# Kernel optimization log

Measured on AMD Instinct MI355X. Metric: run time of the kernel, lower is better.

## Reference

```python
import jax, jax.numpy as jnp
import numpy as np

CODEBOOK_SIZE = 1024
D_MODEL = 512
NUM_SAMPLES = 10
TEMP = 1.0
COMMITMENT_COST = 0.25
PADDING_IDX = 0


def setup_inputs() -> dict:
    key = jax.random.key(0)
    k1, k2, k3 = jax.random.split(key, 3)
    inputs = jax.random.normal(k1, (64, 512, D_MODEL), dtype=jnp.float32)
    padding_mask = jax.random.randint(k2, (64, 512), 0, 2) == 1
    codebook_weight = 0.02 * jax.random.normal(k3, (CODEBOOK_SIZE, D_MODEL), dtype=jnp.float32)
    codebook_weight = codebook_weight.at[PADDING_IDX].set(0.0)  # padding_idx row zeroed
    return {"inputs": inputs, "padding_mask": padding_mask, "codebook_weight": codebook_weight}


def reference(inputs, padding_mask, codebook_weight):
    B, S, D = inputs.shape
    K = codebook_weight.shape[0]
    flat = inputs.reshape(-1, D)  # [N, D]
    # squared-euclidean distances to codebook entries: [N, K]
    dist = (jnp.sum(flat * flat, axis=1, keepdims=True)
            + jnp.sum(codebook_weight * codebook_weight, axis=1)
            - 2.0 * (flat @ codebook_weight.T))
    pad = padding_mask.reshape(-1)  # [N]
    col = jnp.arange(K)
    # padded rows: only code 0 allowed; non-padded rows: code 0 disallowed
    allowed = jnp.where(pad[:, None], col == 0, col != 0)
    dist = jnp.where(allowed, dist, jnp.inf)

    # Multinomial(total_count=NUM_SAMPLES, logits=-dist/TEMP): draw NUM_SAMPLES
    # categorical samples per row and count them.
    logits = -dist / TEMP
    N = flat.shape[0]
    draws = jax.random.categorical(jax.random.key(42), logits, axis=-1,
                                   shape=(NUM_SAMPLES, N))  # [num_samples, N]
    row_idx = jnp.broadcast_to(jnp.arange(N)[None, :], draws.shape)
    samples = jnp.zeros((N, K), jnp.float32).at[row_idx, draws].add(1.0)  # counts, [N, K]

    quantized = (samples @ codebook_weight).reshape(B, S, D) / NUM_SAMPLES

    num_nonpad = (jnp.sum(~pad) * D).astype(jnp.float32)
    e_latent_loss = jnp.sum((jax.lax.stop_gradient(quantized) - inputs) ** 2) / num_nonpad
    loss = COMMITMENT_COST * e_latent_loss

    # straight-through estimator
    quantized_st = inputs + jax.lax.stop_gradient(quantized - inputs)

    avg_probs = jnp.mean(samples, axis=0) / NUM_SAMPLES  # [K]
    perplexity = jnp.exp(-jnp.sum(avg_probs * jnp.log(avg_probs + 1e-10)))

    samples_out = samples.reshape(B, S, K)
    return quantized_st, samples_out, loss, perplexity
```

## Files before the change

kernel.cpp:

```cpp
#include <hip/hip_runtime.h>
#include <stdint.h>

#define NROWS 32768
#define KC 1024
#define DM 512
#define NKPROD 33554432u

typedef _Float16 v8h __attribute__((ext_vector_type(8)));
typedef float v4f __attribute__((ext_vector_type(4)));

__device__ __forceinline__ uint32_t rotl32(uint32_t x, int d) {
  return __builtin_amdgcn_alignbit(x, x, 32 - d);
}

__device__ __forceinline__ void threefry_x2(uint32_t xa, uint32_t xb,
                                            uint32_t& oa, uint32_t& ob) {
  const uint32_t ks1 = 42u, ks2 = 0x1BD11BF0u;
  uint32_t a0 = 0u, a1 = xa + ks1;
  uint32_t b0 = 0u, b1 = xb + ks1;
#define R2(r) { a0 += a1; b0 += b1; a1 = rotl32(a1, r); b1 = rotl32(b1, r); a1 ^= a0; b1 ^= b0; }
  R2(13) R2(15) R2(26) R2(6)
  a0 += ks1; b0 += ks1; a1 += ks2 + 1u; b1 += ks2 + 1u;
  R2(17) R2(29) R2(16) R2(24)
  a0 += ks2; b0 += ks2; a1 += 2u; b1 += 2u;
  R2(13) R2(15) R2(26) R2(6)
  a1 += ks1 + 3u; b1 += ks1 + 3u;
  R2(17) R2(29) R2(16) R2(24)
  a0 += ks1; b0 += ks1; a1 += ks2 + 4u; b1 += ks2 + 4u;
  R2(13) R2(15) R2(26) R2(6)
  a0 += ks2; b0 += ks2; a1 += 5u; b1 += 5u;
#undef R2
  oa = a0 ^ a1;
  ob = b0 ^ b1;
}

__global__ __launch_bounds__(1024) void k_prep(const void* __restrict__ mv,
                                               uint8_t* __restrict__ wm,
                                               int* __restrict__ idx,
                                               int* __restrict__ npp) {
  __shared__ uint32_t sflag;
  __shared__ int scnt[1024];
  int t = threadIdx.x;
  if (t == 0) sflag = 0;
  __syncthreads();
  const uint8_t* mb = (const uint8_t*)mv;
  uint32_t f = 0;
  for (int i = t; i < NROWS; i += 1024)
    if ((i & 3) && mb[i]) f = 1;
  if (f) atomicOr(&sflag, 1u);
  __syncthreads();
  bool isbool = sflag != 0;

  int r0 = t * 32;
  int cnt = 0;
  for (int i = 0; i < 32; ++i) {
    int r = r0 + i;
    bool p = isbool ? (mb[r] != 0) : (((const int*)mv)[r] != 0);
    wm[r] = p ? 1u : 0u;
    cnt += p ? 0 : 1;
  }
  scnt[t] = cnt;
  __syncthreads();
  for (int off = 1; off < 1024; off <<= 1) {
    int v = (t >= off) ? scnt[t - off] : 0;
    __syncthreads();
    scnt[t] += v;
    __syncthreads();
  }
  int NPtot = scnt[1023];
  int pos  = scnt[t] - cnt;
  int ppos = NPtot + (r0 - pos);
  for (int i = 0; i < 32; ++i) {
    int r = r0 + i;
    bool p = isbool ? (mb[r] != 0) : (((const int*)mv)[r] != 0);
    if (!p) idx[pos++] = r; else idx[ppos++] = r;
  }
  if (t == 1023) *npp = NPtot;
}

__global__ __launch_bounds__(256) void k_bsplit(const float* __restrict__ B,
                                                _Float16* __restrict__ Bh2,
                                                _Float16* __restrict__ Bl2,
                                                float* __restrict__ Bn) {
  int k = blockIdx.x * 4 + (threadIdx.x >> 6);
  int l = threadIdx.x & 63;
  const float* bp = B + (size_t)k * DM + l * 8;
  float x[8];
  *(float4*)&x[0] = *(const float4*)bp;
  *(float4*)&x[4] = *(const float4*)(bp + 4);
  _Float16 h[8], lo[8];
  float s = 0.f;
#pragma unroll
  for (int i = 0; i < 8; ++i) {
    _Float16 hh = (_Float16)x[i];
    h[i] = hh; lo[i] = (_Float16)(x[i] - (float)hh);
    s = fmaf(x[i], x[i], s);
  }
  *(v8h*)&Bh2[(size_t)k * DM + l * 8] = *(v8h*)h;
  *(v8h*)&Bl2[(size_t)k * DM + l * 8] = *(v8h*)lo;
#pragma unroll
  for (int off = 32; off; off >>= 1) s += __shfl_xor(s, off, 64);
  if (l == 0) Bn[k] = s;
}

#define LDK 40
__global__ __launch_bounds__(256) void k_gemm3(const float* __restrict__ A,
                                               const _Float16* __restrict__ Bh2,
                                               const _Float16* __restrict__ Bl2,
                                               const float* __restrict__ Bn,
                                               const int* __restrict__ idx,
                                               const int* __restrict__ npp,
                                               float* __restrict__ S) {
  int NP = *npp;
  int bx = blockIdx.x & 7;
  int by = blockIdx.x >> 3;
  int r0 = by * 128, c0 = bx * 128;
  if (r0 >= NP) return;

  __shared__ _Float16 Ah[128 * LDK], Al[128 * LDK];
  __shared__ _Float16 Bh[128 * LDK], Bl[128 * LDK];
  __shared__ float rs[128];
  __shared__ float cs[128];
  __shared__ float tmp[256];

  int tid = threadIdx.x;
  int wid = tid >> 6;
  int wr = wid >> 1, wc = wid & 1;
  int l = tid & 63;
  int lr = l & 15;
  int k8 = (l >> 4) * 8;

  int srow = tid >> 1;
  int ssub = (tid & 1) * 16;

  int orig = idx[r0 + srow];
  const float* ag = A + (size_t)orig * DM + ssub;
  const _Float16* bhg = Bh2 + (size_t)(c0 + srow) * DM + ssub;
  const _Float16* blg = Bl2 + (size_t)(c0 + srow) * DM + ssub;

  if (tid < 128) cs[tid] = Bn[c0 + tid];

  v4f acc[4][4];
#pragma unroll
  for (int m = 0; m < 4; ++m)
#pragma unroll
    for (int n = 0; n < 4; ++n) acc[m][n] = (v4f)0.0f;

  float sqa = 0.f;

  for (int k0 = 0; k0 < DM; k0 += 32) {
    float xa[16];
#pragma unroll
    for (int i = 0; i < 16; i += 4)
      *(float4*)&xa[i] = *(const float4*)(ag + k0 + i);
    v8h bh0 = *(const v8h*)(bhg + k0);
    v8h bh1 = *(const v8h*)(bhg + k0 + 8);
    v8h bl0 = *(const v8h*)(blg + k0);
    v8h bl1 = *(const v8h*)(blg + k0 + 8);
    _Float16 ha[16], la[16];
#pragma unroll
    for (int i = 0; i < 16; ++i) {
      float x = xa[i];
      _Float16 h = (_Float16)x;
      ha[i] = h; la[i] = (_Float16)(x - (float)h);
      sqa = fmaf(x, x, sqa);
    }
    __syncthreads();
    int wb = srow * LDK + ssub;
    *(v8h*)&Ah[wb]     = *(v8h*)&ha[0];
    *(v8h*)&Ah[wb + 8] = *(v8h*)&ha[8];
    *(v8h*)&Al[wb]     = *(v8h*)&la[0];
    *(v8h*)&Al[wb + 8] = *(v8h*)&la[8];
    *(v8h*)&Bh[wb]     = bh0;
    *(v8h*)&Bh[wb + 8] = bh1;
    *(v8h*)&Bl[wb]     = bl0;
    *(v8h*)&Bl[wb + 8] = bl1;
    __syncthreads();

    v8h fah[4], fal[4];
#pragma unroll
    for (int m = 0; m < 4; ++m) {
      int row = wr * 64 + m * 16 + lr;
      fah[m] = *(const v8h*)&Ah[row * LDK + k8];
      fal[m] = *(const v8h*)&Al[row * LDK + k8];
    }
#pragma unroll
    for (int n = 0; n < 4; ++n) {
      int col = wc * 64 + n * 16 + lr;
      v8h fbh = *(const v8h*)&Bh[col * LDK + k8];
      v8h fbl = *(const v8h*)&Bl[col * LDK + k8];
#pragma unroll
      for (int m = 0; m < 4; ++m) {
        acc[m][n] = __builtin_amdgcn_mfma_f32_16x16x32_f16(fah[m], fbh, acc[m][n], 0, 0, 0);
        acc[m][n] = __builtin_amdgcn_mfma_f32_16x16x32_f16(fah[m], fbl, acc[m][n], 0, 0, 0);
        acc[m][n] = __builtin_amdgcn_mfma_f32_16x16x32_f16(fal[m], fbh, acc[m][n], 0, 0, 0);
      }
    }
  }

  tmp[tid] = sqa;
  __syncthreads();
  if ((tid & 1) == 0) rs[srow] = tmp[tid] + tmp[tid + 1];
  __syncthreads();

  float cnp[4];
#pragma unroll
  for (int n = 0; n < 4; ++n) cnp[n] = cs[wc * 64 + n * 16 + lr];

#pragma unroll
  for (int m = 0; m < 4; ++m) {
    int rl = wr * 64 + m * 16 + (l >> 4) * 4;
#pragma unroll
    for (int r = 0; r < 4; ++r) {
      int org = idx[r0 + rl + r];
      float rq = rs[rl + r];
      float* sp = S + (size_t)org * KC + c0;
#pragma unroll
      for (int n = 0; n < 4; ++n) {
        int cl = wc * 64 + n * 16 + lr;
        sp[cl] = -((rq + cnp[n]) - 2.0f * acc[m][n][r]);
      }
    }
  }
}

__global__ __launch_bounds__(256, 8) void k_sample_f(
    const float* __restrict__ S, const float* __restrict__ X,
    const float* __restrict__ CW, const int* __restrict__ idx,
    const int* __restrict__ npp,
    float* __restrict__ qout, float* __restrict__ sout,
    float* __restrict__ cnt, double* __restrict__ esum) {
  int NP = *npp;
  int slot = blockIdx.x * 4 + (threadIdx.x >> 6);
  int l = threadIdx.x & 63;
  int n = idx[slot];
  int base = l * 16;

  if (slot >= NP) {
    float* so = sout + (size_t)n * KC + base;
    float4 z = make_float4(0.f, 0.f, 0.f, 0.f);
    *(float4*)(so)      = (l == 0) ? make_float4(10.f, 0.f, 0.f, 0.f) : z;
    *(float4*)(so + 4)  = z;
    *(float4*)(so + 8)  = z;
    *(float4*)(so + 12) = z;
    const float* xr = X + (size_t)n * DM + l * 8;
    float4 x0 = *(const float4*)xr, x1 = *(const float4*)(xr + 4);
    float* qo = qout + (size_t)n * DM + l * 8;
    *(float4*)qo       = z;
    *(float4*)(qo + 4) = z;
    double ls = (double)(x0.x*x0.x) + (double)(x0.y*x0.y)
              + (double)(x0.z*x0.z) + (double)(x0.w*x0.w)
              + (double)(x1.x*x1.x) + (double)(x1.y*x1.y)
              + (double)(x1.z*x1.z) + (double)(x1.w*x1.w);
#pragma unroll
    for (int off = 32; off; off >>= 1) ls += __shfl_xor(ls, off, 64);
    if (l == 0) atomicAdd(&esum[n & 63], ls);
    return;
  }

  const float* srow = S + (size_t)n * KC + base;

  float lmax;
  {
    float lg0[16];
#pragma unroll
    for (int j = 0; j < 16; j += 4)
      *(float4*)&lg0[j] = *(const float4*)(srow + j);
    if (l == 0) lg0[0] = -__builtin_inff();
    lmax = lg0[0];
#pragma unroll
    for (int i = 1; i < 16; ++i) lmax = fmaxf(lmax, lg0[i]);
#pragma unroll
    for (int off = 32; off; off >>= 1)
      lmax = fmaxf(lmax, __shfl_xor(lmax, off, 64));
  }

  float bv[10];
  uint32_t bi[10];
#pragma unroll
  for (int s = 0; s < 10; ++s) { bv[s] = -__builtin_inff(); bi[s] = 0xFFFFFFFFu; }

  uint32_t tb0 = (uint32_t)n * (uint32_t)KC + (uint32_t)base;
#pragma unroll 1
  for (int j = 0; j < 16; ++j) {
    float lgj = srow[j];
    uint32_t kk = (uint32_t)(base + j);
    if (kk == 0u) lgj = -__builtin_inff();
    float mj = 0.69314718056f * __expf(lmax - lgj);
    uint32_t t0 = tb0 + (uint32_t)j;
#pragma unroll
    for (int sp = 0; sp < 5; ++sp) {
      uint32_t ba, bb;
      threefry_x2(t0 + (uint32_t)(2 * sp) * NKPROD,
                  t0 + (uint32_t)(2 * sp + 1) * NKPROD, ba, bb);
      float fa = __uint_as_float((ba >> 9) | 0x3F800000u) - 1.0f;
      float fb = __uint_as_float((bb >> 9) | 0x3F800000u) - 1.0f;
      float ua = fmaxf(1.17549435e-38f, fa);
      float ub = fmaxf(1.17549435e-38f, fb);
      float va = __log2f(ua) * mj;
      float vb = __log2f(ub) * mj;
      if (va > bv[2 * sp])     { bv[2 * sp] = va;     bi[2 * sp] = kk; }
      if (vb > bv[2 * sp + 1]) { bv[2 * sp + 1] = vb; bi[2 * sp + 1] = kk; }
    }
  }

#pragma unroll
  for (int s = 0; s < 10; ++s) {
#pragma unroll
    for (int off = 32; off; off >>= 1) {
      float ov = __shfl_xor(bv[s], off, 64);
      uint32_t oi = __shfl_xor(bi[s], off, 64);
      if (ov > bv[s] || (ov == bv[s] && oi < bi[s])) { bv[s] = ov; bi[s] = oi; }
    }
  }

  float* so = sout + (size_t)n * KC + base;
#pragma unroll
  for (int j4 = 0; j4 < 16; j4 += 4) {
    float c[4];
#pragma unroll
    for (int i = 0; i < 4; ++i) {
      uint32_t k = (uint32_t)(base + j4 + i);
      float cc = 0.f;
#pragma unroll
      for (int s = 0; s < 10; ++s) cc += (bi[s] == k) ? 1.f : 0.f;
      c[i] = cc;
    }
    *(float4*)(so + j4) = make_float4(c[0], c[1], c[2], c[3]);
  }

  float q[8];
#pragma unroll
  for (int i = 0; i < 8; ++i) q[i] = 0.f;
#pragma unroll
  for (int s = 0; s < 10; ++s) {
    const float* cr = CW + (size_t)bi[s] * DM + l * 8;
    float4 g0 = *(const float4*)cr;
    float4 g1 = *(const float4*)(cr + 4);
    q[0] += g0.x; q[1] += g0.y; q[2] += g0.z; q[3] += g0.w;
    q[4] += g1.x; q[5] += g1.y; q[6] += g1.z; q[7] += g1.w;
    if (l == 0) atomicAdd(&cnt[bi[s]], 1.0f);
  }

  const float* xr = X + (size_t)n * DM + l * 8;
  float4 x0 = *(const float4*)xr, x1 = *(const float4*)(xr + 4);
  float xs[8] = {x0.x, x0.y, x0.z, x0.w, x1.x, x1.y, x1.z, x1.w};
  float st[8];
  double ls = 0.0;
#pragma unroll
  for (int j = 0; j < 8; ++j) {
    float qq = q[j] / 10.0f;
    float d = qq - xs[j];
    ls += (double)(d * d);
    st[j] = xs[j] + d;
  }
  float* qo = qout + (size_t)n * DM + l * 8;
  *(float4*)qo       = make_float4(st[0], st[1], st[2], st[3]);
  *(float4*)(qo + 4) = make_float4(st[4], st[5], st[6], st[7]);

#pragma unroll
  for (int off = 32; off; off >>= 1) ls += __shfl_xor(ls, off, 64);
  if (l == 0) atomicAdd(&esum[n & 63], ls);
}

__global__ __launch_bounds__(256) void k_final(const uint8_t* __restrict__ wm,
                                               const float* __restrict__ cnt,
                                               const double* __restrict__ esum,
                                               float* __restrict__ scal) {
  __shared__ int sni[256];
  __shared__ double snd[256];
  int t = threadIdx.x;
  int np = 0;
  for (int i = t; i < NROWS; i += 256) np += wm[i];
  sni[t] = np;
  __syncthreads();
  for (int off = 128; off; off >>= 1) {
    if (t < off) sni[t] += sni[t + off];
    __syncthreads();
  }
  int npad = sni[0];
  double ss = 0.0;
  for (int k = t; k < KC; k += 256) {
    float c = (k == 0) ? (float)(npad * 10) : cnt[k];
    float p = c / 327680.0f;
    ss += (double)(p * logf(p + 1e-10f));
  }
  snd[t] = ss;
  __syncthreads();
  for (int off = 128; off; off >>= 1) {
    if (t < off) snd[t] += snd[t + off];
    __syncthreads();
  }
  if (t == 0) {
    double es = 0.0;
    for (int i = 0; i < 64; ++i) es += esum[i];
    float num_nonpad = (float)((NROWS - npad) * DM);
    float el = (float)es / num_nonpad;
    scal[0] = 0.25f * el;
    scal[1] = expf(-(float)snd[0]);
  }
}

extern "C" void kernel_launch(void* const* d_in, const int* in_sizes, int n_in,
                              void* d_out, int out_size, void* d_ws, size_t ws_size,
                              hipStream_t stream) {
  const float* X  = (const float*)d_in[0];
  const void*  M  = d_in[1];
  const float* CW = (const float*)d_in[2];
  float* out  = (float*)d_out;
  float* qout = out;
  float* sout = out + 16777216;
  float* scal = out + 50331648;
  _Float16* Bh2 = (_Float16*)qout;
  _Float16* Bl2 = (_Float16*)(qout + 262144);
  float*    Bn  = qout + 524288;
  uint8_t* ws = (uint8_t*)d_ws;
  double*   esum = (double*)ws;
  int*      npp  = (int*)(ws + 512);
  float*    cnt  = (float*)(ws + 1024);
  uint8_t*  wm   = ws + 16384;
  int*      idx  = (int*)(ws + 49152);
  (void)in_sizes; (void)n_in; (void)out_size; (void)ws_size;

  hipMemsetAsync(d_ws, 0, 8192, stream);
  k_prep<<<1, 1024, 0, stream>>>(M, wm, idx, npp);
  k_bsplit<<<256, 256, 0, stream>>>(CW, Bh2, Bl2, Bn);
  k_gemm3<<<2048, 256, 0, stream>>>(X, Bh2, Bl2, Bn, idx, npp, sout);
  k_sample_f<<<8192, 256, 0, stream>>>(sout, X, CW, idx, npp, qout, sout, cnt, esum);
  k_final<<<1, 256, 0, stream>>>(wm, cnt, esum, scal);
}
```

Before: 576.3 us.

## Fuse codebook split into prep kernel and move padded-row work into idle GEMM blocks

```diff
diff --git a/kernel.cpp b/kernel.cpp
--- a/kernel.cpp
+++ b/kernel.cpp
@@ -34,10 +34,37 @@
   ob = b0 ^ b1;
 }
 
-__global__ __launch_bounds__(1024) void k_prep(const void* __restrict__ mv,
-                                               uint8_t* __restrict__ wm,
-                                               int* __restrict__ idx,
-                                               int* __restrict__ npp) {
+__global__ __launch_bounds__(1024) void k_prep_b(const void* __restrict__ mv,
+                                                 const float* __restrict__ B,
+                                                 uint8_t* __restrict__ wm,
+                                                 int* __restrict__ idx,
+                                                 int* __restrict__ npp,
+                                                 _Float16* __restrict__ Bh2,
+                                                 _Float16* __restrict__ Bl2,
+                                                 float* __restrict__ Bn) {
+  if (blockIdx.x > 0) {
+    int k = (blockIdx.x - 1) * 16 + (threadIdx.x >> 6);
+    int l = threadIdx.x & 63;
+    const float* bp = B + (size_t)k * DM + l * 8;
+    float x[8];
+    *(float4*)&x[0] = *(const float4*)bp;
+    *(float4*)&x[4] = *(const float4*)(bp + 4);
+    _Float16 h[8], lo[8];
+    float s = 0.f;
+#pragma unroll
+    for (int i = 0; i < 8; ++i) {
+      _Float16 hh = (_Float16)x[i];
+      h[i] = hh; lo[i] = (_Float16)(x[i] - (float)hh);
+      s = fmaf(x[i], x[i], s);
+    }
+    *(v8h*)&Bh2[(size_t)k * DM + l * 8] = *(v8h*)h;
+    *(v8h*)&Bl2[(size_t)k * DM + l * 8] = *(v8h*)lo;
+#pragma unroll
+    for (int off = 32; off; off >>= 1) s += __shfl_xor(s, off, 64);
+    if (l == 0) Bn[k] = s;
+    return;
+  }
+
   __shared__ uint32_t sflag;
   __shared__ int scnt[1024];
   int t = threadIdx.x;
@@ -78,44 +105,51 @@
   if (t == 1023) *npp = NPtot;
 }
 
-__global__ __launch_bounds__(256) void k_bsplit(const float* __restrict__ B,
-                                                _Float16* __restrict__ Bh2,
-                                                _Float16* __restrict__ Bl2,
-                                                float* __restrict__ Bn) {
-  int k = blockIdx.x * 4 + (threadIdx.x >> 6);
-  int l = threadIdx.x & 63;
-  const float* bp = B + (size_t)k * DM + l * 8;
-  float x[8];
-  *(float4*)&x[0] = *(const float4*)bp;
-  *(float4*)&x[4] = *(const float4*)(bp + 4);
-  _Float16 h[8], lo[8];
-  float s = 0.f;
-#pragma unroll
-  for (int i = 0; i < 8; ++i) {
-    _Float16 hh = (_Float16)x[i];
-    h[i] = hh; lo[i] = (_Float16)(x[i] - (float)hh);
-    s = fmaf(x[i], x[i], s);
-  }
-  *(v8h*)&Bh2[(size_t)k * DM + l * 8] = *(v8h*)h;
-  *(v8h*)&Bl2[(size_t)k * DM + l * 8] = *(v8h*)lo;
-#pragma unroll
-  for (int off = 32; off; off >>= 1) s += __shfl_xor(s, off, 64);
-  if (l == 0) Bn[k] = s;
-}
-
 #define LDK 40
-__global__ __launch_bounds__(256) void k_gemm3(const float* __restrict__ A,
+__global__ __launch_bounds__(256) void k_gemm4(const float* __restrict__ A,
                                                const _Float16* __restrict__ Bh2,
                                                const _Float16* __restrict__ Bl2,
                                                const float* __restrict__ Bn,
                                                const int* __restrict__ idx,
                                                const int* __restrict__ npp,
-                                               float* __restrict__ S) {
+                                               float* __restrict__ S,
+                                               double* __restrict__ esum) {
   int NP = *npp;
+  int ngroups = (NP + 127) >> 7;
   int bx = blockIdx.x & 7;
   int by = blockIdx.x >> 3;
-  int r0 = by * 128, c0 = bx * 128;
-  if (r0 >= NP) return;
+  int tid = threadIdx.x;
+
+  if (by >= ngroups) {
+    int pbase = ngroups << 7;
+    int pcount = NROWS - pbase;
+    if (pcount <= 0) return;
+    int nidle = (256 - ngroups) * 8;
+    int iidx = (by - ngroups) * 8 + bx;
+    int chunk = (pcount + nidle - 1) / nidle;
+    int s0 = pbase + iidx * chunk;
+    int s1 = s0 + chunk; if (s1 > NROWS) s1 = NROWS;
+    int wid = tid >> 6, l = tid & 63;
+    for (int s = s0 + wid; s < s1; s += 4) {
+      int n = idx[s];
+      float* so = S + (size_t)n * KC + l * 16;
+      float4 z = make_float4(0.f, 0.f, 0.f, 0.f);
+      *(float4*)(so)      = (l == 0) ? make_float4(10.f, 0.f, 0.f, 0.f) : z;
+      *(float4*)(so + 4)  = z;
+      *(float4*)(so + 8)  = z;
+      *(float4*)(so + 12) = z;
+      const float* xr = A + (size_t)n * DM + l * 8;
+      float4 x0 = *(const float4*)xr, x1 = *(const float4*)(xr + 4);
+      double ls = (double)(x0.x*x0.x) + (double)(x0.y*x0.y)
+                + (double)(x0.z*x0.z) + (double)(x0.w*x0.w)
+                + (double)(x1.x*x1.x) + (double)(x1.y*x1.y)
+                + (double)(x1.z*x1.z) + (double)(x1.w*x1.w);
+#pragma unroll
+      for (int off = 32; off; off >>= 1) ls += __shfl_xor(ls, off, 64);
+      if (l == 0) atomicAdd(&esum[n & 63], ls);
+    }
+    return;
+  }
 
   __shared__ _Float16 Ah[128 * LDK], Al[128 * LDK];
   __shared__ _Float16 Bh[128 * LDK], Bl[128 * LDK];
@@ -123,7 +157,7 @@
   __shared__ float cs[128];
   __shared__ float tmp[256];
 
-  int tid = threadIdx.x;
+  int r0 = by * 128, c0 = bx * 128;
   int wid = tid >> 6;
   int wr = wid >> 1, wc = wid & 1;
   int l = tid & 63;
@@ -224,7 +258,7 @@
   }
 }
 
-__global__ __launch_bounds__(256, 8) void k_sample_f(
+__global__ __launch_bounds__(256, 8) void k_sample_g(
     const float* __restrict__ S, const float* __restrict__ X,
     const float* __restrict__ CW, const int* __restrict__ idx,
     const int* __restrict__ npp,
@@ -237,24 +271,27 @@
   int base = l * 16;
 
   if (slot >= NP) {
-    float* so = sout + (size_t)n * KC + base;
     float4 z = make_float4(0.f, 0.f, 0.f, 0.f);
-    *(float4*)(so)      = (l == 0) ? make_float4(10.f, 0.f, 0.f, 0.f) : z;
-    *(float4*)(so + 4)  = z;
-    *(float4*)(so + 8)  = z;
-    *(float4*)(so + 12) = z;
-    const float* xr = X + (size_t)n * DM + l * 8;
-    float4 x0 = *(const float4*)xr, x1 = *(const float4*)(xr + 4);
     float* qo = qout + (size_t)n * DM + l * 8;
     *(float4*)qo       = z;
     *(float4*)(qo + 4) = z;
-    double ls = (double)(x0.x*x0.x) + (double)(x0.y*x0.y)
-              + (double)(x0.z*x0.z) + (double)(x0.w*x0.w)
-              + (double)(x1.x*x1.x) + (double)(x1.y*x1.y)
-              + (double)(x1.z*x1.z) + (double)(x1.w*x1.w);
-#pragma unroll
-    for (int off = 32; off; off >>= 1) ls += __shfl_xor(ls, off, 64);
-    if (l == 0) atomicAdd(&esum[n & 63], ls);
+    int ngroups = (NP + 127) >> 7;
+    if (slot < (ngroups << 7)) {
+      float* so = sout + (size_t)n * KC + base;
+      *(float4*)(so)      = (l == 0) ? make_float4(10.f, 0.f, 0.f, 0.f) : z;
+      *(float4*)(so + 4)  = z;
+      *(float4*)(so + 8)  = z;
+      *(float4*)(so + 12) = z;
+      const float* xr = X + (size_t)n * DM + l * 8;
+      float4 x0 = *(const float4*)xr, x1 = *(const float4*)(xr + 4);
+      double ls = (double)(x0.x*x0.x) + (double)(x0.y*x0.y)
+                + (double)(x0.z*x0.z) + (double)(x0.w*x0.w)
+                + (double)(x1.x*x1.x) + (double)(x1.y*x1.y)
+                + (double)(x1.z*x1.z) + (double)(x1.w*x1.w);
+#pragma unroll
+      for (int off = 32; off; off >>= 1) ls += __shfl_xor(ls, off, 64);
+      if (l == 0) atomicAdd(&esum[n & 63], ls);
+    }
     return;
   }
 
@@ -395,7 +432,8 @@
     double es = 0.0;
     for (int i = 0; i < 64; ++i) es += esum[i];
     float num_nonpad = (float)((NROWS - npad) * DM);
-    float el = (float)es / num_nonpad;
+    float el = (float)(*esum == *esum ? es : es) / num_nonpad;
+    el = (float)es / num_nonpad;
     scal[0] = 0.25f * el;
     scal[1] = expf(-(float)snd[0]);
   }
@@ -423,9 +461,8 @@
   (void)in_sizes; (void)n_in; (void)out_size; (void)ws_size;
 
   hipMemsetAsync(d_ws, 0, 8192, stream);
-  k_prep<<<1, 1024, 0, stream>>>(M, wm, idx, npp);
-  k_bsplit<<<256, 256, 0, stream>>>(CW, Bh2, Bl2, Bn);
-  k_gemm3<<<2048, 256, 0, stream>>>(X, Bh2, Bl2, Bn, idx, npp, sout);
-  k_sample_f<<<8192, 256, 0, stream>>>(sout, X, CW, idx, npp, qout, sout, cnt, esum);
+  k_prep_b<<<65, 1024, 0, stream>>>(M, CW, wm, idx, npp, Bh2, Bl2, Bn);
+  k_gemm4<<<2048, 256, 0, stream>>>(X, Bh2, Bl2, Bn, idx, npp, sout, esum);
+  k_sample_g<<<8192, 256, 0, stream>>>(sout, X, CW, idx, npp, qout, sout, cnt, esum);
   k_final<<<1, 256, 0, stream>>>(wm, cnt, esum, scal);
 }
```

After: 593.1 us. 2.9% more time.

## Parallelize mask compaction and pre-split inputs to fp16 hi/lo before GEMM

Applied to the files above, without the earlier changes.

```diff
diff --git a/kernel.cpp b/kernel.cpp
--- a/kernel.cpp
+++ b/kernel.cpp
@@ -34,48 +34,100 @@
   ob = b0 ^ b1;
 }
 
-__global__ __launch_bounds__(1024) void k_prep(const void* __restrict__ mv,
-                                               uint8_t* __restrict__ wm,
-                                               int* __restrict__ idx,
-                                               int* __restrict__ npp) {
-  __shared__ uint32_t sflag;
-  __shared__ int scnt[1024];
-  int t = threadIdx.x;
-  if (t == 0) sflag = 0;
+__global__ __launch_bounds__(256) void k_count(const uint8_t* __restrict__ mb,
+                                               uint32_t* __restrict__ flag,
+                                               int* __restrict__ cntB,
+                                               int* __restrict__ cntI) {
+  __shared__ int sB[256], sI[256];
+  int t = threadIdx.x, b = blockIdx.x;
+  int T = b * 256 + t;
+  uint32_t f = 0;
+#pragma unroll
+  for (int i = 0; i < 2; ++i) {
+    int bi = T * 2 + i;
+    if ((bi & 3) && mb[bi]) f = 1;
+  }
+  if (f) atomicOr(flag, 1u);
+  const int* mi = (const int*)mb;
+  int r0 = b * 512 + t * 2;
+  int cB = 0, cI = 0;
+#pragma unroll
+  for (int i = 0; i < 2; ++i) {
+    int r = r0 + i;
+    cB += (mb[r] == 0) ? 1 : 0;
+    cI += (mi[r] == 0) ? 1 : 0;
+  }
+  sB[t] = cB; sI[t] = cI;
   __syncthreads();
-  const uint8_t* mb = (const uint8_t*)mv;
-  uint32_t f = 0;
-  for (int i = t; i < NROWS; i += 1024)
-    if ((i & 3) && mb[i]) f = 1;
-  if (f) atomicOr(&sflag, 1u);
+  for (int off = 128; off; off >>= 1) {
+    if (t < off) { sB[t] += sB[t + off]; sI[t] += sI[t + off]; }
+    __syncthreads();
+  }
+  if (t == 0) { cntB[b] = sB[0]; cntI[b] = sI[0]; }
+}
+
+__global__ __launch_bounds__(256) void k_scatter(const uint8_t* __restrict__ mb,
+                                                 const uint32_t* __restrict__ flag,
+                                                 const int* __restrict__ cntB,
+                                                 const int* __restrict__ cntI,
+                                                 int* __restrict__ idx,
+                                                 int* __restrict__ npp) {
+  __shared__ int sc[256];
+  int t = threadIdx.x, b = blockIdx.x;
+  bool isbool = (*flag) != 0;
+  const int* mi = (const int*)mb;
+  const int* cnt = isbool ? cntB : cntI;
+  int pre = 0, tot = 0;
+  for (int j = 0; j < 64; ++j) {
+    int c = cnt[j];
+    if (j < b) pre += c;
+    tot += c;
+  }
+  int r0 = b * 512 + t * 2;
+  bool np0 = isbool ? (mb[r0] == 0)     : (mi[r0] == 0);
+  bool np1 = isbool ? (mb[r0 + 1] == 0) : (mi[r0 + 1] == 0);
+  int my = (int)np0 + (int)np1;
+  sc[t] = my;
   __syncthreads();
-  bool isbool = sflag != 0;
-
-  int r0 = t * 32;
-  int cnt = 0;
-  for (int i = 0; i < 32; ++i) {
-    int r = r0 + i;
-    bool p = isbool ? (mb[r] != 0) : (((const int*)mv)[r] != 0);
-    wm[r] = p ? 1u : 0u;
-    cnt += p ? 0 : 1;
-  }
-  scnt[t] = cnt;
-  __syncthreads();
-  for (int off = 1; off < 1024; off <<= 1) {
-    int v = (t >= off) ? scnt[t - off] : 0;
-    __syncthreads();
-    scnt[t] += v;
-    __syncthreads();
-  }
-  int NPtot = scnt[1023];
-  int pos  = scnt[t] - cnt;
-  int ppos = NPtot + (r0 - pos);
-  for (int i = 0; i < 32; ++i) {
-    int r = r0 + i;
-    bool p = isbool ? (mb[r] != 0) : (((const int*)mv)[r] != 0);
-    if (!p) idx[pos++] = r; else idx[ppos++] = r;
-  }
-  if (t == 1023) *npp = NPtot;
+  for (int off = 1; off < 256; off <<= 1) {
+    int v = (t >= off) ? sc[t - off] : 0;
+    __syncthreads();
+    sc[t] += v;
+    __syncthreads();
+  }
+  int excl = sc[t] - my;
+  int npPos = pre + excl;
+  int padPos = tot + (b * 512 - pre) + (t * 2 - excl);
+  if (np0) idx[npPos++] = r0;     else idx[padPos++] = r0;
+  if (np1) idx[npPos]   = r0 + 1; else idx[padPos]   = r0 + 1;
+  if (b == 0 && t == 0) *npp = tot;
+}
+
+__global__ __launch_bounds__(256) void k_asplit(const float* __restrict__ A,
+                                                const int* __restrict__ idx,
+                                                _Float16* __restrict__ Ah2,
+                                                _Float16* __restrict__ Al2,
+                                                float* __restrict__ An) {
+  int slot = blockIdx.x * 4 + (threadIdx.x >> 6);
+  int l = threadIdx.x & 63;
+  int n = idx[slot];
+  const float* ap = A + (size_t)n * DM + l * 8;
+  float x[8];
+  *(float4*)&x[0] = *(const float4*)ap;
+  *(float4*)&x[4] = *(const float4*)(ap + 4);
+  _Float16 h[8], lo[8];
+  float s = 0.f;
+#pragma unroll
+  for (int i = 0; i < 8; ++i) {
+    _Float16 hh = (_Float16)x[i];
+    h[i] = hh; lo[i] = (_Float16)(x[i] - (float)hh);
+    s = fmaf(x[i], x[i], s);
+  }
+  *(v8h*)&Ah2[(size_t)slot * DM + l * 8] = *(v8h*)h;
+  *(v8h*)&Al2[(size_t)slot * DM + l * 8] = *(v8h*)lo;
+#pragma unroll
+  for (int off = 32; off; off >>= 1) s += __shfl_xor(s, off, 64);
+  if (l == 0) An[slot] = s;
 }
 
 __global__ __launch_bounds__(256) void k_bsplit(const float* __restrict__ B,
@@ -104,7 +156,9 @@
 }
 
 #define LDK 40
-__global__ __launch_bounds__(256) void k_gemm3(const float* __restrict__ A,
+__global__ __launch_bounds__(256) void k_gemm5(const _Float16* __restrict__ Ah2,
+                                               const _Float16* __restrict__ Al2,
+                                               const float* __restrict__ An,
                                                const _Float16* __restrict__ Bh2,
                                                const _Float16* __restrict__ Bl2,
                                                const float* __restrict__ Bn,
@@ -119,9 +173,6 @@
 
   __shared__ _Float16 Ah[128 * LDK], Al[128 * LDK];
   __shared__ _Float16 Bh[128 * LDK], Bl[128 * LDK];
-  __shared__ float rs[128];
-  __shared__ float cs[128];
-  __shared__ float tmp[256];
 
   int tid = threadIdx.x;
   int wid = tid >> 6;
@@ -133,44 +184,32 @@
   int srow = tid >> 1;
   int ssub = (tid & 1) * 16;
 
-  int orig = idx[r0 + srow];
-  const float* ag = A + (size_t)orig * DM + ssub;
+  const _Float16* ahg = Ah2 + (size_t)(r0 + srow) * DM + ssub;
+  const _Float16* alg = Al2 + (size_t)(r0 + srow) * DM + ssub;
   const _Float16* bhg = Bh2 + (size_t)(c0 + srow) * DM + ssub;
   const _Float16* blg = Bl2 + (size_t)(c0 + srow) * DM + ssub;
 
-  if (tid < 128) cs[tid] = Bn[c0 + tid];
-
   v4f acc[4][4];
 #pragma unroll
   for (int m = 0; m < 4; ++m)
 #pragma unroll
     for (int n = 0; n < 4; ++n) acc[m][n] = (v4f)0.0f;
 
-  float sqa = 0.f;
-
   for (int k0 = 0; k0 < DM; k0 += 32) {
-    float xa[16];
-#pragma unroll
-    for (int i = 0; i < 16; i += 4)
-      *(float4*)&xa[i] = *(const float4*)(ag + k0 + i);
+    v8h ah0 = *(const v8h*)(ahg + k0);
+    v8h ah1 = *(const v8h*)(ahg + k0 + 8);
+    v8h al0 = *(const v8h*)(alg + k0);
+    v8h al1 = *(const v8h*)(alg + k0 + 8);
     v8h bh0 = *(const v8h*)(bhg + k0);
     v8h bh1 = *(const v8h*)(bhg + k0 + 8);
     v8h bl0 = *(const v8h*)(blg + k0);
     v8h bl1 = *(const v8h*)(blg + k0 + 8);
-    _Float16 ha[16], la[16];
-#pragma unroll
-    for (int i = 0; i < 16; ++i) {
-      float x = xa[i];
-      _Float16 h = (_Float16)x;
-      ha[i] = h; la[i] = (_Float16)(x - (float)h);
-      sqa = fmaf(x, x, sqa);
-    }
     __syncthreads();
     int wb = srow * LDK + ssub;
-    *(v8h*)&Ah[wb]     = *(v8h*)&ha[0];
-    *(v8h*)&Ah[wb + 8] = *(v8h*)&ha[8];
-    *(v8h*)&Al[wb]     = *(v8h*)&la[0];
-    *(v8h*)&Al[wb + 8] = *(v8h*)&la[8];
+    *(v8h*)&Ah[wb]     = ah0;
+    *(v8h*)&Ah[wb + 8] = ah1;
+    *(v8h*)&Al[wb]     = al0;
+    *(v8h*)&Al[wb + 8] = al1;
     *(v8h*)&Bh[wb]     = bh0;
     *(v8h*)&Bh[wb + 8] = bh1;
     *(v8h*)&Bl[wb]     = bl0;
@@ -198,14 +237,9 @@
     }
   }
 
-  tmp[tid] = sqa;
-  __syncthreads();
-  if ((tid & 1) == 0) rs[srow] = tmp[tid] + tmp[tid + 1];
-  __syncthreads();
-
   float cnp[4];
 #pragma unroll
-  for (int n = 0; n < 4; ++n) cnp[n] = cs[wc * 64 + n * 16 + lr];
+  for (int n = 0; n < 4; ++n) cnp[n] = Bn[c0 + wc * 64 + n * 16 + lr];
 
 #pragma unroll
   for (int m = 0; m < 4; ++m) {
@@ -213,7 +247,7 @@
 #pragma unroll
     for (int r = 0; r < 4; ++r) {
       int org = idx[r0 + rl + r];
-      float rq = rs[rl + r];
+      float rq = An[r0 + rl + r];
       float* sp = S + (size_t)org * KC + c0;
 #pragma unroll
       for (int n = 0; n < 4; ++n) {
@@ -224,7 +258,40 @@
   }
 }
 
-__global__ __launch_bounds__(256, 8) void k_sample_f(
+__global__ __launch_bounds__(256) void k_pad(const float* __restrict__ X,
+                                             const int* __restrict__ idx,
+                                             const int* __restrict__ npp,
+                                             float* __restrict__ qout,
+                                             float* __restrict__ sout,
+                                             double* __restrict__ esum) {
+  int NP = *npp;
+  int slot = blockIdx.x * 4 + (threadIdx.x >> 6);
+  if (slot < NP) return;
+  int n = idx[slot];
+  int l = threadIdx.x & 63;
+
+  float* so = sout + (size_t)n * KC + l * 16;
+  float4 z = make_float4(0.f, 0.f, 0.f, 0.f);
+  *(float4*)(so)      = (l == 0) ? make_float4(10.f, 0.f, 0.f, 0.f) : z;
+  *(float4*)(so + 4)  = z;
+  *(float4*)(so + 8)  = z;
+  *(float4*)(so + 12) = z;
+
+  const float* xr = X + (size_t)n * DM + l * 8;
+  float4 x0 = *(const float4*)xr, x1 = *(const float4*)(xr + 4);
+  float* qo = qout + (size_t)n * DM + l * 8;
+  *(float4*)qo       = z;
+  *(float4*)(qo + 4) = z;
+  double ls = (double)(x0.x*x0.x) + (double)(x0.y*x0.y)
+            + (double)(x0.z*x0.z) + (double)(x0.w*x0.w)
+            + (double)(x1.x*x1.x) + (double)(x1.y*x1.y)
+            + (double)(x1.z*x1.z) + (double)(x1.w*x1.w);
+#pragma unroll
+  for (int off = 32; off; off >>= 1) ls += __shfl_xor(ls, off, 64);
+  if (l == 0) atomicAdd(&esum[n & 63], ls);
+}
+
+__global__ __launch_bounds__(256, 8) void k_sample_i(
     const float* __restrict__ S, const float* __restrict__ X,
     const float* __restrict__ CW, const int* __restrict__ idx,
     const int* __restrict__ npp,
@@ -232,32 +299,10 @@
     float* __restrict__ cnt, double* __restrict__ esum) {
   int NP = *npp;
   int slot = blockIdx.x * 4 + (threadIdx.x >> 6);
+  if (slot >= NP) return;
+  int n = idx[slot];
   int l = threadIdx.x & 63;
-  int n = idx[slot];
   int base = l * 16;
-
-  if (slot >= NP) {
-    float* so = sout + (size_t)n * KC + base;
-    float4 z = make_float4(0.f, 0.f, 0.f, 0.f);
-    *(float4*)(so)      = (l == 0) ? make_float4(10.f, 0.f, 0.f, 0.f) : z;
-    *(float4*)(so + 4)  = z;
-    *(float4*)(so + 8)  = z;
-    *(float4*)(so + 12) = z;
-    const float* xr = X + (size_t)n * DM + l * 8;
-    float4 x0 = *(const float4*)xr, x1 = *(const float4*)(xr + 4);
-    float* qo = qout + (size_t)n * DM + l * 8;
-    *(float4*)qo       = z;
-    *(float4*)(qo + 4) = z;
-    double ls = (double)(x0.x*x0.x) + (double)(x0.y*x0.y)
-              + (double)(x0.z*x0.z) + (double)(x0.w*x0.w)
-              + (double)(x1.x*x1.x) + (double)(x1.y*x1.y)
-              + (double)(x1.z*x1.z) + (double)(x1.w*x1.w);
-#pragma unroll
-    for (int off = 32; off; off >>= 1) ls += __shfl_xor(ls, off, 64);
-    if (l == 0) atomicAdd(&esum[n & 63], ls);
-    return;
-  }
-
   const float* srow = S + (size_t)n * KC + base;
 
   float lmax;
@@ -363,22 +408,13 @@
   if (l == 0) atomicAdd(&esum[n & 63], ls);
 }
 
-__global__ __launch_bounds__(256) void k_final(const uint8_t* __restrict__ wm,
+__global__ __launch_bounds__(256) void k_final(const int* __restrict__ npp,
                                                const float* __restrict__ cnt,
                                                const double* __restrict__ esum,
                                                float* __restrict__ scal) {
-  __shared__ int sni[256];
   __shared__ double snd[256];
   int t = threadIdx.x;
-  int np = 0;
-  for (int i = t; i < NROWS; i += 256) np += wm[i];
-  sni[t] = np;
-  __syncthreads();
-  for (int off = 128; off; off >>= 1) {
-    if (t < off) sni[t] += sni[t + off];
-    __syncthreads();
-  }
-  int npad = sni[0];
+  int npad = NROWS - *npp;
   double ss = 0.0;
   for (int k = t; k < KC; k += 256) {
     float c = (k == 0) ? (float)(npad * 10) : cnt[k];
@@ -411,21 +447,29 @@
   float* qout = out;
   float* sout = out + 16777216;
   float* scal = out + 50331648;
-  _Float16* Bh2 = (_Float16*)qout;
-  _Float16* Bl2 = (_Float16*)(qout + 262144);
-  float*    Bn  = qout + 524288;
+  _Float16* Ah2 = (_Float16*)qout;
+  _Float16* Al2 = Ah2 + 16777216;
   uint8_t* ws = (uint8_t*)d_ws;
   double*   esum = (double*)ws;
-  int*      npp  = (int*)(ws + 512);
+  uint32_t* flag = (uint32_t*)(ws + 512);
+  int*      npp  = (int*)(ws + 768);
   float*    cnt  = (float*)(ws + 1024);
-  uint8_t*  wm   = ws + 16384;
-  int*      idx  = (int*)(ws + 49152);
+  int*      cntB = (int*)(ws + 5120);
+  int*      cntI = (int*)(ws + 5376);
+  int*      idx  = (int*)(ws + 8192);
+  float*    An   = (float*)(ws + 139264);
+  _Float16* Bh2  = (_Float16*)(ws + 270336);
+  _Float16* Bl2  = (_Float16*)(ws + 270336 + 1048576);
+  float*    Bn   = (float*)(ws + 270336 + 2097152);
   (void)in_sizes; (void)n_in; (void)out_size; (void)ws_size;
 
   hipMemsetAsync(d_ws, 0, 8192, stream);
-  k_prep<<<1, 1024, 0, stream>>>(M, wm, idx, npp);
+  k_count<<<64, 256, 0, stream>>>((const uint8_t*)M, flag, cntB, cntI);
+  k_scatter<<<64, 256, 0, stream>>>((const uint8_t*)M, flag, cntB, cntI, idx, npp);
+  k_asplit<<<8192, 256, 0, stream>>>(X, idx, Ah2, Al2, An);
   k_bsplit<<<256, 256, 0, stream>>>(CW, Bh2, Bl2, Bn);
-  k_gemm3<<<2048, 256, 0, stream>>>(X, Bh2, Bl2, Bn, idx, npp, sout);
-  k_sample_f<<<8192, 256, 0, stream>>>(sout, X, CW, idx, npp, qout, sout, cnt, esum);
-  k_final<<<1, 256, 0, stream>>>(wm, cnt, esum, scal);
-}
+  k_gemm5<<<2048, 256, 0, stream>>>(Ah2, Al2, An, Bh2, Bl2, Bn, idx, npp, sout);
+  k_pad<<<8192, 256, 0, stream>>>(X, idx, npp, qout, sout, esum);
+  k_sample_i<<<8192, 256, 0, stream>>>(sout, X, CW, idx, npp, qout, sout, cnt, esum);
+  k_final<<<1, 256, 0, stream>>>(npp, cnt, esum, scal);
+}
```

Measured after the change: 508.7 us. 11.7% less time.
